# Performance work log

Measured on AMD Instinct MI355X. Metric: run time of the kernel, lower is better.

## Reference

```python
import jax, jax.numpy as jnp
import numpy as np

NUM_EXPERTS = 8
INTER = 2816   # moe_intermediate_size
DIM = 1024
T = 16         # flattened tokens
A = 2          # top-k experts per token


def setup_inputs() -> dict:
    key = jax.random.key(0)
    k_x, k_idx, k1, k2, k3 = jax.random.split(key, 5)
    x = jax.random.normal(k_x, (T, DIM), dtype=jnp.float32)
    expert_indices = jax.random.randint(k_idx, (T, A), 0, NUM_EXPERTS, dtype=jnp.int64)
    scale = 0.02
    w1 = jax.random.normal(k1, (NUM_EXPERTS, INTER, DIM), dtype=jnp.float32) * scale
    w2 = jax.random.normal(k2, (NUM_EXPERTS, DIM, INTER), dtype=jnp.float32) * scale
    w3 = jax.random.normal(k3, (NUM_EXPERTS, INTER, DIM), dtype=jnp.float32) * scale
    return {"x": x, "expert_indices": expert_indices, "w1": w1, "w2": w2, "w3": w3}


def reference(x, expert_indices, w1, w2, w3):
    # Gather per-token expert weights (same access pattern as the torch module).
    w1_g = w1[expert_indices]  # [T, A, INTER, DIM]
    w3_g = w3[expert_indices]  # [T, A, INTER, DIM]
    w2_g = w2[expert_indices]  # [T, A, DIM, INTER]
    # SwiGLU: silu(x @ w1^T) * (x @ w3^T), then project back with w2.
    x1 = jax.nn.silu(jnp.einsum('ti,taoi->tao', x, w1_g))  # [T, A, INTER]
    x3 = jnp.einsum('ti,taoi->tao', x, w3_g)               # [T, A, INTER]
    expert_outs = jnp.einsum('tao,taio->tai', x1 * x3, w2_g)  # [T, A, DIM]
    return expert_outs
```

## Files before the change

kernel.cpp:

```cpp
#include <hip/hip_runtime.h>
#include <math.h>

#define TOK   16
#define TOPA  2
#define NPAIR (TOK * TOPA)
#define DIM   1024
#define INTER 2816
#define NEXP  8

#define R1 2
#define R2 2

__device__ inline unsigned pair_mask(const int* __restrict__ eidx, int e) {
    unsigned mask = 0;
    #pragma unroll
    for (int k = 0; k < NPAIR / 4; ++k) {
        const int4 v = ((const int4*)eidx)[k];
        mask |= (unsigned)(v.x == e) << (4 * k + 0);
        mask |= (unsigned)(v.y == e) << (4 * k + 1);
        mask |= (unsigned)(v.z == e) << (4 * k + 2);
        mask |= (unsigned)(v.w == e) << (4 * k + 3);
    }
    return mask;
}

__global__ __launch_bounds__(256) void moe_gate_up(
    const float* __restrict__ x,
    const int*   __restrict__ eidx,
    const float* __restrict__ w1,
    const float* __restrict__ w3,
    float*       __restrict__ h)
{
    const int e    = blockIdx.y;
    const int tid  = threadIdx.x;
    const int lane = tid & 63;
    const int wave = tid >> 6;

    unsigned mask = pair_mask(eidx, e);
    if (!mask) return;

    const int o0 = blockIdx.x * (4 * R1) + wave * R1;
    const float* w1b = w1 + ((size_t)e * INTER + o0) * DIM;
    const float* w3b = w3 + ((size_t)e * INTER + o0) * DIM;

    float4 wa[R1][4], wb[R1][4];
    #pragma unroll
    for (int r = 0; r < R1; ++r) {
        #pragma unroll
        for (int k = 0; k < 4; ++k) {
            wa[r][k] = ((const float4*)(w1b + (size_t)r * DIM))[k * 64 + lane];
            wb[r][k] = ((const float4*)(w3b + (size_t)r * DIM))[k * 64 + lane];
        }
    }

    while (mask) {
        const int p = __builtin_ctz(mask);
        mask &= mask - 1;
        const int t = p >> 1;

        const float* xr = x + (size_t)t * DIM;
        float4 xv[4];
        #pragma unroll
        for (int k = 0; k < 4; ++k)
            xv[k] = ((const float4*)xr)[k * 64 + lane];

        float s1[R1], s3[R1];
        #pragma unroll
        for (int r = 0; r < R1; ++r) { s1[r] = 0.f; s3[r] = 0.f; }
        #pragma unroll
        for (int k = 0; k < 4; ++k) {
            #pragma unroll
            for (int r = 0; r < R1; ++r) {
                s1[r] += wa[r][k].x * xv[k].x + wa[r][k].y * xv[k].y
                       + wa[r][k].z * xv[k].z + wa[r][k].w * xv[k].w;
                s3[r] += wb[r][k].x * xv[k].x + wb[r][k].y * xv[k].y
                       + wb[r][k].z * xv[k].z + wb[r][k].w * xv[k].w;
            }
        }

        #pragma unroll
        for (int off = 32; off > 0; off >>= 1) {
            #pragma unroll
            for (int r = 0; r < R1; ++r) {
                s1[r] += __shfl_xor(s1[r], off);
                s3[r] += __shfl_xor(s3[r], off);
            }
        }

        if (lane == 0) {
            #pragma unroll
            for (int r = 0; r < R1; ++r) {
                const float g = s1[r] / (1.f + __expf(-s1[r]));
                h[(size_t)p * INTER + o0 + r] = g * s3[r];
            }
        }
    }
}

__global__ __launch_bounds__(256) void moe_down(
    const float* __restrict__ h,
    const int*   __restrict__ eidx,
    const float* __restrict__ w2,
    float*       __restrict__ out)
{
    const int e    = blockIdx.y;
    const int tid  = threadIdx.x;
    const int lane = tid & 63;
    const int wave = tid >> 6;

    unsigned mask = pair_mask(eidx, e);
    if (!mask) return;

    const int d0 = blockIdx.x * (4 * R2) + wave * R2;
    const float* w2b = w2 + ((size_t)e * DIM + d0) * INTER;

    float4 wv[R2][11];
    #pragma unroll
    for (int r = 0; r < R2; ++r) {
        #pragma unroll
        for (int k = 0; k < 11; ++k)
            wv[r][k] = ((const float4*)(w2b + (size_t)r * INTER))[k * 64 + lane];
    }

    while (mask) {
        const int p = __builtin_ctz(mask);
        mask &= mask - 1;

        const float* hr = h + (size_t)p * INTER;
        float s[R2];
        #pragma unroll
        for (int r = 0; r < R2; ++r) s[r] = 0.f;

        #pragma unroll
        for (int k = 0; k < 11; ++k) {
            const float4 hv = ((const float4*)hr)[k * 64 + lane];
            #pragma unroll
            for (int r = 0; r < R2; ++r) {
                s[r] += wv[r][k].x * hv.x + wv[r][k].y * hv.y
                      + wv[r][k].z * hv.z + wv[r][k].w * hv.w;
            }
        }

        #pragma unroll
        for (int off = 32; off > 0; off >>= 1) {
            #pragma unroll
            for (int r = 0; r < R2; ++r)
                s[r] += __shfl_xor(s[r], off);
        }

        if (lane == 0) {
            #pragma unroll
            for (int r = 0; r < R2; ++r)
                out[(size_t)p * DIM + d0 + r] = s[r];
        }
    }
}

extern "C" void kernel_launch(void* const* d_in, const int* in_sizes, int n_in,
                              void* d_out, int out_size, void* d_ws, size_t ws_size,
                              hipStream_t stream) {
    const float* x    = (const float*)d_in[0];
    const int*   eidx = (const int*)  d_in[1];
    const float* w1   = (const float*)d_in[2];
    const float* w2   = (const float*)d_in[3];
    const float* w3   = (const float*)d_in[4];
    float* out = (float*)d_out;
    float* h   = (float*)d_ws;

    dim3 g1(INTER / (4 * R1), NEXP);
    moe_gate_up<<<g1, 256, 0, stream>>>(x, eidx, w1, w3, h);

    dim3 g2(DIM / (4 * R2), NEXP);
    moe_down<<<g2, 256, 0, stream>>>(h, eidx, w2, out);
}
```

Baseline: 59.53 us.

## Stream MoE weights through double-buffered LDS with direct global-to-LDS loads

Both kernels now cover more rows per block (32 gate/up rows, 16 down rows). Weights and activations are streamed in K-chunks into double-buffered shared memory using global_load_lds, with swizzled layouts and explicit waitcnt/barrier pipelining. Up to 8 token-pairs per expert are processed together from the staged tiles, replacing per-wave register-held weights and a full 64-lane shuffle reduction for each pair. The aim is to overlap memory transfers with compute and use memory bandwidth better, at the cost of more barriers, fewer blocks, and more complex synchronisation.

```diff
diff --git a/kernel.cpp b/kernel.cpp
--- a/kernel.cpp
+++ b/kernel.cpp
@@ -1,17 +1,37 @@
 #include <hip/hip_runtime.h>
 #include <math.h>
+#include <stdint.h>
 
 #define TOK   16
 #define TOPA  2
-#define NPAIR (TOK * TOPA)
+#define NPAIR 32
 #define DIM   1024
 #define INTER 2816
 #define NEXP  8
 
-#define R1 2
-#define R2 2
-
-__device__ inline unsigned pair_mask(const int* __restrict__ eidx, int e) {
+#define KC1   64
+#define NC1   16
+#define GROWS 32
+#define KC2   128
+#define NC2   22
+#define DROWS 16
+
+#define WAITV(n) asm volatile("s_waitcnt vmcnt(" #n ")" ::: "memory")
+#define BARR()   do { __builtin_amdgcn_s_barrier(); __builtin_amdgcn_sched_barrier(0); } while (0)
+
+__device__ __forceinline__ float dot4(float4 a, float4 b) {
+    return a.x * b.x + a.y * b.y + a.z * b.z + a.w * b.w;
+}
+
+__device__ __forceinline__ void gload16(const float* g, float* l) {
+    auto gp = reinterpret_cast<const __attribute__((address_space(1))) uint32_t*>(
+                  reinterpret_cast<uintptr_t>(g));
+    auto lp = reinterpret_cast<__attribute__((address_space(3))) uint32_t*>(
+                  reinterpret_cast<uintptr_t>(l));
+    __builtin_amdgcn_global_load_lds(gp, lp, 16, 0, 0);
+}
+
+__device__ __forceinline__ unsigned pair_mask(const int* __restrict__ eidx, int e) {
     unsigned mask = 0;
     #pragma unroll
     for (int k = 0; k < NPAIR / 4; ++k) {
@@ -24,135 +44,219 @@
     return mask;
 }
 
+template <int JMAX>
+__device__ __forceinline__ void gate_group(
+    const float* __restrict__ w1, const float* __restrict__ w3,
+    const float* __restrict__ x,  float* __restrict__ hout,
+    float* wb0, float* wb1, float* xb0, float* xb1,
+    int e, int r0, int tid, const int (&pj)[8], int npg)
+{
+    const int q2   = tid & 3;
+    const int trow = tid >> 2;
+    const int mt   = trow & 1;
+    const int row  = trow >> 1;
+
+    const float* wsrc[4];
+    #pragma unroll
+    for (int q = 0; q < 4; ++q) {
+        const int flat  = q * 256 + tid;
+        const int strow = flat >> 4;
+        const int scol  = (flat & 15) ^ (strow & 7);
+        const float* wbase = (strow & 1) ? w3 : w1;
+        wsrc[q] = wbase + ((size_t)e * INTER + r0 + (strow >> 1)) * DIM + scol * 4;
+    }
+    const float* xsrc = x + (size_t)(tid >> 4) * DIM + (tid & 15) * 4;
+
+    int tb[JMAX];
+    #pragma unroll
+    for (int j = 0; j < JMAX; ++j) tb[j] = (pj[j] >> 1) * KC1;
+
+    float acc[JMAX];
+    #pragma unroll
+    for (int j = 0; j < JMAX; ++j) acc[j] = 0.f;
+
+    auto stage = [&](int kc, float* wb, float* xb) {
+        const int ko = kc * KC1;
+        #pragma unroll
+        for (int q = 0; q < 4; ++q)
+            gload16(wsrc[q] + ko, wb + q * 1024 + tid * 4);
+        gload16(xsrc + ko, xb + tid * 4);
+    };
+    auto compute = [&](const float* wb, const float* xb) {
+        #pragma unroll
+        for (int kq = 0; kq < 4; ++kq) {
+            const int q16 = (q2 << 2) | kq;
+            const float4 w4 =
+                *(const float4*)(wb + trow * KC1 + ((q16 ^ (trow & 7)) << 2));
+            #pragma unroll
+            for (int j = 0; j < JMAX; ++j) {
+                const float4 xv = *(const float4*)(xb + tb[j] + (q16 << 2));
+                acc[j] += dot4(w4, xv);
+            }
+        }
+    };
+
+    stage(0, wb0, xb0);
+    #pragma unroll 1
+    for (int c = 0; c < NC1; c += 2) {
+        stage(c + 1, wb1, xb1);
+        WAITV(5);
+        BARR();
+        compute(wb0, xb0);
+        BARR();
+        if (c + 2 < NC1) { stage(c + 2, wb0, xb0); WAITV(5); }
+        else             { WAITV(0); }
+        BARR();
+        compute(wb1, xb1);
+        BARR();
+    }
+
+    #pragma unroll
+    for (int j = 0; j < JMAX; ++j) {
+        float s = acc[j];
+        s += __shfl_xor(s, 1);
+        s += __shfl_xor(s, 2);
+        const float part = __shfl_xor(s, 4);
+        if (mt == 0 && (j & 3) == q2 && j < npg) {
+            const float g = s / (1.f + __expf(-s));
+            hout[(size_t)pj[j] * INTER + r0 + row] = g * part;
+        }
+    }
+}
+
 __global__ __launch_bounds__(256) void moe_gate_up(
-    const float* __restrict__ x,
-    const int*   __restrict__ eidx,
-    const float* __restrict__ w1,
-    const float* __restrict__ w3,
-    float*       __restrict__ h)
-{
-    const int e    = blockIdx.y;
-    const int tid  = threadIdx.x;
-    const int lane = tid & 63;
-    const int wave = tid >> 6;
-
-    unsigned mask = pair_mask(eidx, e);
-    if (!mask) return;
-
-    const int o0 = blockIdx.x * (4 * R1) + wave * R1;
-    const float* w1b = w1 + ((size_t)e * INTER + o0) * DIM;
-    const float* w3b = w3 + ((size_t)e * INTER + o0) * DIM;
-
-    float4 wa[R1][4], wb[R1][4];
-    #pragma unroll
-    for (int r = 0; r < R1; ++r) {
-        #pragma unroll
-        for (int k = 0; k < 4; ++k) {
-            wa[r][k] = ((const float4*)(w1b + (size_t)r * DIM))[k * 64 + lane];
-            wb[r][k] = ((const float4*)(w3b + (size_t)r * DIM))[k * 64 + lane];
-        }
-    }
-
-    while (mask) {
-        const int p = __builtin_ctz(mask);
-        mask &= mask - 1;
-        const int t = p >> 1;
-
-        const float* xr = x + (size_t)t * DIM;
-        float4 xv[4];
-        #pragma unroll
-        for (int k = 0; k < 4; ++k)
-            xv[k] = ((const float4*)xr)[k * 64 + lane];
-
-        float s1[R1], s3[R1];
-        #pragma unroll
-        for (int r = 0; r < R1; ++r) { s1[r] = 0.f; s3[r] = 0.f; }
-        #pragma unroll
-        for (int k = 0; k < 4; ++k) {
+    const float* __restrict__ x,  const int* __restrict__ eidx,
+    const float* __restrict__ w1, const float* __restrict__ w3,
+    float* __restrict__ hout)
+{
+    __shared__ float wb0[4096], wb1[4096];
+    __shared__ float xb0[1024], xb1[1024];
+
+    const int e = blockIdx.y;
+    unsigned mrem = pair_mask(eidx, e);
+    if (!mrem) return;
+
+    const int tid = threadIdx.x;
+    const int r0  = blockIdx.x * GROWS;
+
+    while (mrem) {
+        int pj[8];
+        const int pfirst = __builtin_ctz(mrem);
+        unsigned mg = mrem;
+        int npg = 0;
+        #pragma unroll
+        for (int j = 0; j < 8; ++j) {
+            if (mg) { pj[j] = __builtin_ctz(mg); mg &= mg - 1; ++npg; }
+            else    { pj[j] = pfirst; }
+        }
+        mrem = mg;
+        if (npg > 4) gate_group<8>(w1, w3, x, hout, wb0, wb1, xb0, xb1, e, r0, tid, pj, npg);
+        else         gate_group<4>(w1, w3, x, hout, wb0, wb1, xb0, xb1, e, r0, tid, pj, npg);
+    }
+}
+
+template <int JMAX>
+__device__ __forceinline__ void down_group(
+    const float* __restrict__ hsrcbase, const float* __restrict__ w2,
+    float* __restrict__ outp,
+    float* wb0, float* wb1, float* hb0, float* hb1,
+    int e, int r0, int tid, const int (&pj)[8], int npg)
+{
+    const int sub  = tid & 15;
+    const int slot = tid >> 4;
+
+    const float* wsrc[2];
+    #pragma unroll
+    for (int q = 0; q < 2; ++q) {
+        const int flat  = q * 256 + tid;
+        const int strow = flat >> 5;
+        const int scol  = (flat & 31) ^ (strow & 7);
+        wsrc[q] = w2 + ((size_t)e * DIM + r0 + strow) * INTER + scol * 4;
+    }
+    const int hr = tid >> 5;
+    int hp = pj[0];
+    #pragma unroll
+    for (int j = 1; j < 8; ++j) if (hr == j) hp = pj[j];
+    const float* hsrc = hsrcbase + (size_t)hp * INTER + (tid & 31) * 4;
+
+    float acc[JMAX];
+    #pragma unroll
+    for (int j = 0; j < JMAX; ++j) acc[j] = 0.f;
+
+    auto stage = [&](int kc, float* wb, float* hb) {
+        const int ko = kc * KC2;
+        gload16(wsrc[0] + ko, wb + tid * 4);
+        gload16(wsrc[1] + ko, wb + 1024 + tid * 4);
+        gload16(hsrc + ko, hb + tid * 4);
+    };
+    auto compute = [&](const float* wb, const float* hb) {
+        #pragma unroll
+        for (int qq = 0; qq < 2; ++qq) {
+            const int q32 = (sub << 1) | qq;
+            const float4 w4 =
+                *(const float4*)(wb + slot * KC2 + ((q32 ^ (slot & 7)) << 2));
             #pragma unroll
-            for (int r = 0; r < R1; ++r) {
-                s1[r] += wa[r][k].x * xv[k].x + wa[r][k].y * xv[k].y
-                       + wa[r][k].z * xv[k].z + wa[r][k].w * xv[k].w;
-                s3[r] += wb[r][k].x * xv[k].x + wb[r][k].y * xv[k].y
-                       + wb[r][k].z * xv[k].z + wb[r][k].w * xv[k].w;
+            for (int j = 0; j < JMAX; ++j) {
+                const float4 hv = *(const float4*)(hb + j * KC2 + (q32 << 2));
+                acc[j] += dot4(w4, hv);
             }
         }
-
-        #pragma unroll
-        for (int off = 32; off > 0; off >>= 1) {
-            #pragma unroll
-            for (int r = 0; r < R1; ++r) {
-                s1[r] += __shfl_xor(s1[r], off);
-                s3[r] += __shfl_xor(s3[r], off);
-            }
-        }
-
-        if (lane == 0) {
-            #pragma unroll
-            for (int r = 0; r < R1; ++r) {
-                const float g = s1[r] / (1.f + __expf(-s1[r]));
-                h[(size_t)p * INTER + o0 + r] = g * s3[r];
-            }
-        }
+    };
+
+    stage(0, wb0, hb0);
+    #pragma unroll 1
+    for (int c = 0; c < NC2; c += 2) {
+        stage(c + 1, wb1, hb1);
+        WAITV(3);
+        BARR();
+        compute(wb0, hb0);
+        BARR();
+        if (c + 2 < NC2) { stage(c + 2, wb0, hb0); WAITV(3); }
+        else             { WAITV(0); }
+        BARR();
+        compute(wb1, hb1);
+        BARR();
+    }
+
+    #pragma unroll
+    for (int j = 0; j < JMAX; ++j) {
+        float s = acc[j];
+        s += __shfl_xor(s, 1);
+        s += __shfl_xor(s, 2);
+        s += __shfl_xor(s, 4);
+        s += __shfl_xor(s, 8);
+        if (sub == j && j < npg)
+            outp[(size_t)pj[j] * DIM + r0 + slot] = s;
     }
 }
 
 __global__ __launch_bounds__(256) void moe_down(
-    const float* __restrict__ h,
-    const int*   __restrict__ eidx,
-    const float* __restrict__ w2,
-    float*       __restrict__ out)
-{
-    const int e    = blockIdx.y;
-    const int tid  = threadIdx.x;
-    const int lane = tid & 63;
-    const int wave = tid >> 6;
-
-    unsigned mask = pair_mask(eidx, e);
-    if (!mask) return;
-
-    const int d0 = blockIdx.x * (4 * R2) + wave * R2;
-    const float* w2b = w2 + ((size_t)e * DIM + d0) * INTER;
-
-    float4 wv[R2][11];
-    #pragma unroll
-    for (int r = 0; r < R2; ++r) {
-        #pragma unroll
-        for (int k = 0; k < 11; ++k)
-            wv[r][k] = ((const float4*)(w2b + (size_t)r * INTER))[k * 64 + lane];
-    }
-
-    while (mask) {
-        const int p = __builtin_ctz(mask);
-        mask &= mask - 1;
-
-        const float* hr = h + (size_t)p * INTER;
-        float s[R2];
-        #pragma unroll
-        for (int r = 0; r < R2; ++r) s[r] = 0.f;
-
-        #pragma unroll
-        for (int k = 0; k < 11; ++k) {
-            const float4 hv = ((const float4*)hr)[k * 64 + lane];
-            #pragma unroll
-            for (int r = 0; r < R2; ++r) {
-                s[r] += wv[r][k].x * hv.x + wv[r][k].y * hv.y
-                      + wv[r][k].z * hv.z + wv[r][k].w * hv.w;
-            }
-        }
-
-        #pragma unroll
-        for (int off = 32; off > 0; off >>= 1) {
-            #pragma unroll
-            for (int r = 0; r < R2; ++r)
-                s[r] += __shfl_xor(s[r], off);
-        }
-
-        if (lane == 0) {
-            #pragma unroll
-            for (int r = 0; r < R2; ++r)
-                out[(size_t)p * DIM + d0 + r] = s[r];
-        }
+    const float* __restrict__ h, const int* __restrict__ eidx,
+    const float* __restrict__ w2, float* __restrict__ outp)
+{
+    __shared__ float wb0[2048], wb1[2048];
+    __shared__ float hb0[1024], hb1[1024];
+
+    const int e = blockIdx.y;
+    unsigned mrem = pair_mask(eidx, e);
+    if (!mrem) return;
+
+    const int tid = threadIdx.x;
+    const int r0  = blockIdx.x * DROWS;
+
+    while (mrem) {
+        int pj[8];
+        const int pfirst = __builtin_ctz(mrem);
+        unsigned mg = mrem;
+        int npg = 0;
+        #pragma unroll
+        for (int j = 0; j < 8; ++j) {
+            if (mg) { pj[j] = __builtin_ctz(mg); mg &= mg - 1; ++npg; }
+            else    { pj[j] = pfirst; }
+        }
+        mrem = mg;
+        if (npg > 4) down_group<8>(h, w2, outp, wb0, wb1, hb0, hb1, e, r0, tid, pj, npg);
+        else         down_group<4>(h, w2, outp, wb0, wb1, hb0, hb1, e, r0, tid, pj, npg);
     }
 }
 
@@ -165,11 +269,11 @@
     const float* w2   = (const float*)d_in[3];
     const float* w3   = (const float*)d_in[4];
     float* out = (float*)d_out;
-    float* h   = (float*)d_ws;
-
-    dim3 g1(INTER / (4 * R1), NEXP);
-    moe_gate_up<<<g1, 256, 0, stream>>>(x, eidx, w1, w3, h);
-
-    dim3 g2(DIM / (4 * R2), NEXP);
-    moe_down<<<g2, 256, 0, stream>>>(h, eidx, w2, out);
-}
+    float* hws = (float*)d_ws;
+
+    dim3 g1(INTER / GROWS, NEXP);
+    moe_gate_up<<<g1, 256, 0, stream>>>(x, eidx, w1, w3, hws);
+
+    dim3 g2(DIM / DROWS, NEXP);
+    moe_down<<<g2, 256, 0, stream>>>(hws, eidx, w2, out);
+}
```

After: 79.91 us. +34.2%, slower.
